# Performance work log

Hardware: AMD Instinct MI355X
Metric: run time of the kernel (lower is better)

## Reference

```python
import jax, jax.numpy as jnp
import numpy as np

NUM_NODES = 1024
K = 16384
G = 128

def setup_inputs() -> dict:
    key = jax.random.key(0)
    k1, k2, k3 = jax.random.split(key, 3)
    x = jax.random.normal(k1, (G, NUM_NODES, 64), dtype=jnp.float32)
    # original draws fresh xavier-uniform embeddings inside forward; we
    # materialize equivalent random embeddings here (only ordering matters).
    emb_s = jax.random.normal(k2, (G, NUM_NODES, 1), dtype=jnp.float32)
    emb_t = jax.random.normal(k3, (G, 1, NUM_NODES), dtype=jnp.float32)
    return {"x": x, "emb_s": emb_s, "emb_t": emb_t}

def reference(x, emb_s, emb_t):
    num_graphs = x.shape[0]
    n = NUM_NODES
    # rank-1 outer product adjacency: [G, N, N]
    adj = emb_s * emb_t  # broadcast (G,N,1)*(G,1,N)
    # mask diagonal with -inf
    diag = jnp.eye(n, dtype=bool)
    adj = jnp.where(diag[None, :, :], -jnp.inf, adj)
    # global top-k over flattened N*N per graph
    adj_flat = adj.reshape(num_graphs, n * n)
    _, indices = jax.lax.top_k(adj_flat, K)  # [G, K]
    # scatter ones at selected positions
    out_flat = jnp.zeros((num_graphs, n * n), dtype=adj.dtype)
    rows = jnp.arange(num_graphs)[:, None]
    out_flat = out_flat.at[rows, indices].set(1.0)
    return out_flat.reshape(num_graphs, n, n)
```

## Files before the change

### kernel.cpp

```cpp
#include <hip/hip_runtime.h>
#include <stdint.h>

#define NNODES 1024
#define NGRAPH 128
#define TOPK   16384
#define EQCAP  4096

typedef float vfloat4 __attribute__((ext_vector_type(4)));

__device__ __forceinline__ uint32_t fkey(float x) {
    uint32_t u = __float_as_uint(x);
    return (u & 0x80000000u) ? ~u : (u | 0x80000000u);
}
__device__ __forceinline__ float inv_fkey(uint32_t k) {
    uint32_t u = (k & 0x80000000u) ? (k & 0x7FFFFFFFu) : ~k;
    return __uint_as_float(u);
}

__global__ __launch_bounds__(NNODES)
void select_kernel(const float* __restrict__ s, const float* __restrict__ t,
                   uint32_t* __restrict__ Tout, uint32_t* __restrict__ Rout,
                   uint32_t* __restrict__ eqCntG, uint32_t* __restrict__ eqIdxG) {
    const int g = blockIdx.x, i = threadIdx.x;
    __shared__ uint64_t spk[NNODES];
    __shared__ float    tvs[NNODES];
    __shared__ uint32_t wsum[16];
    __shared__ uint32_t sLo, sHi, sDir, sEqCnt;
    __shared__ uint32_t sEqList[EQCAP];

    const float tv_i = t[g * NNODES + i];
    spk[i] = ((uint64_t)fkey(tv_i) << 16) | (uint32_t)i;
    if (i == 0) { sLo = 0u; sHi = 0xFFFFFFFFu; sEqCnt = 0u; }

    for (int k = 2; k <= NNODES; k <<= 1) {
        for (int j = k >> 1; j > 0; j >>= 1) {
            __syncthreads();
            int partner = i ^ j;
            if (partner > i) {
                bool asc = ((i & k) == 0);
                uint64_t a = spk[i], b = spk[partner];
                if ((a > b) == asc) { spk[i] = b; spk[partner] = a; }
            }
        }
    }
    __syncthreads();
    tvs[i] = inv_fkey((uint32_t)(spk[i] >> 16));

    const float sv = s[g * NNODES + i];
    const bool sneg = (__float_as_uint(sv) >> 31) != 0;
    const uint32_t kdiag = fkey(sv * tv_i);
    __syncthreads();

    auto srchRange = [&](uint32_t cand, int lo_, int hi_) -> int {
        while (lo_ < hi_) {
            int mid = (lo_ + hi_) >> 1;
            bool pred = fkey(sv * tvs[mid]) > cand;
            bool goLeft = sneg ? !pred : pred;
            if (goLeft) hi_ = mid; else lo_ = mid + 1;
        }
        return lo_;
    };

    int rlo = 0, rhi = NNODES;
    uint32_t cntHi = 0u;

    for (int it = 0; it < 33; ++it) {
        const uint32_t lo = sLo, hi = sHi;
        const uint32_t mid = lo + ((hi - lo) >> 1);
        const int b = srchRange(mid, rlo, rhi);
        uint32_t c = sneg ? (uint32_t)b : (uint32_t)(NNODES - b);
        if (kdiag > mid) c--;
        uint32_t r = c;
        for (int off = 32; off; off >>= 1) r += __shfl_down(r, off);
        if ((i & 63) == 0) wsum[i >> 6] = r;
        __syncthreads();
        if (i == 0 && lo < hi) {
            uint32_t tot = 0;
            for (int w = 0; w < 16; ++w) tot += wsum[w];
            if (tot < TOPK) { sHi = mid; sDir = 0u; cntHi = tot; }
            else            { sLo = mid + 1; sDir = 1u; }
        }
        __syncthreads();
        if (lo < hi) {
            if (sDir == 0u) { if (!sneg) rhi = b; else rlo = b; }
            else            { if (!sneg) rlo = b; else rhi = b; }
        }
    }
    const uint32_t T = sLo;
    if (i == 0) { Tout[g] = T; Rout[g] = TOPK - cntHi; }

    auto bound = [&](bool ge) -> int {
        int lo_ = 0, hi_ = NNODES;
        while (lo_ < hi_) {
            int mid = (lo_ + hi_) >> 1;
            uint32_t k = fkey(sv * tvs[mid]);
            bool pred = ge ? (k >= T) : (k > T);
            bool goLeft = sneg ? !pred : pred;
            if (goLeft) hi_ = mid; else lo_ = mid + 1;
        }
        return lo_;
    };
    int e0, e1;
    if (!sneg) { e0 = bound(true);  e1 = bound(false); }
    else       { e0 = bound(false); e1 = bound(true);  }
    for (int p = e0; p < e1; ++p) {
        uint32_t j = (uint32_t)(spk[p] & 0xFFFFu);
        if ((int)j == i) continue;
        uint32_t slot = atomicAdd(&sEqCnt, 1u);
        if (slot < EQCAP) sEqList[slot] = (uint32_t)(i * NNODES) + j;
    }
    __syncthreads();
    uint32_t E = sEqCnt; if (E > EQCAP) E = EQCAP;
    if (i == 0) eqCntG[g] = E;
    for (uint32_t p = i; p < E; p += NNODES) eqIdxG[g * EQCAP + p] = sEqList[p];
}

__global__ __launch_bounds__(256)
void write_kernel(const float* __restrict__ s, const float* __restrict__ t,
                  const uint32_t* __restrict__ Tin, const uint32_t* __restrict__ Rin,
                  const uint32_t* __restrict__ eqCntG, const uint32_t* __restrict__ eqIdxG,
                  float* __restrict__ out) {
    const int b = blockIdx.x;
    const int g = b >> 10, i = b & 1023;
    const uint32_t T = Tin[g];
    const float sv = s[(size_t)g * NNODES + i];
    const vfloat4 tv = ((const vfloat4*)(t + (size_t)g * NNODES))[threadIdx.x];
    const int j0 = threadIdx.x * 4;
    const uint32_t k0 = fkey(sv * tv.x), k1 = fkey(sv * tv.y);
    const uint32_t k2 = fkey(sv * tv.z), k3 = fkey(sv * tv.w);
    vfloat4 o;
    o.x = (k0 > T && (j0 + 0) != i) ? 1.0f : 0.0f;
    o.y = (k1 > T && (j0 + 1) != i) ? 1.0f : 0.0f;
    o.z = (k2 > T && (j0 + 2) != i) ? 1.0f : 0.0f;
    o.w = (k3 > T && (j0 + 3) != i) ? 1.0f : 0.0f;
    if (k0 == T || k1 == T || k2 == T || k3 == T) {
        uint32_t E = eqCntG[g]; if (E > EQCAP) E = EQCAP;
        const uint32_t R = Rin[g];
        const uint32_t* eq = eqIdxG + (size_t)g * EQCAP;
        const uint32_t kk[4] = {k0, k1, k2, k3};
        #pragma unroll
        for (int q = 0; q < 4; ++q) {
            const uint32_t j = j0 + q;
            if (kk[q] == T && (int)j != i) {
                const uint32_t f = (uint32_t)i * NNODES + j;
                uint32_t rank = 0;
                for (uint32_t e2 = 0; e2 < E; ++e2) rank += (eq[e2] < f) ? 1u : 0u;
                if (rank < R) ((float*)&o)[q] = 1.0f;
            }
        }
    }
    ((vfloat4*)(out + (size_t)g * NNODES * NNODES + (size_t)i * NNODES))[threadIdx.x] = o;
}

extern "C" void kernel_launch(void* const* d_in, const int* in_sizes, int n_in,
                              void* d_out, int out_size, void* d_ws, size_t ws_size,
                              hipStream_t stream) {
    const float* s = (const float*)d_in[1];
    const float* t = (const float*)d_in[2];
    float* out = (float*)d_out;

    char* ws = (char*)d_ws;
    uint32_t* Tbuf  = (uint32_t*)ws; ws += (size_t)NGRAPH * 4;
    uint32_t* Rbuf  = (uint32_t*)ws; ws += (size_t)NGRAPH * 4;
    uint32_t* eqCnt = (uint32_t*)ws; ws += (size_t)NGRAPH * 4;
    uint32_t* eqIdx = (uint32_t*)ws; ws += (size_t)NGRAPH * EQCAP * 4;

    select_kernel<<<NGRAPH, NNODES, 0, stream>>>(s, t, Tbuf, Rbuf, eqCnt, eqIdx);
    write_kernel<<<NGRAPH * NNODES, 256, 0, stream>>>(s, t, Tbuf, Rbuf, eqCnt, eqIdx, out);
}
```

Baseline: 137.2 us.

## Use wave barriers for intra-wave sort stages and narrow threshold search bounds

In the bitonic sort, block-wide __syncthreads is replaced by a wavefront barrier when the compare stride stays within one 64-lane wave. This cuts the number of block-level barriers. The threshold bisection now starts from a tighter range: the lower bound is the minimum over rows of each row's 17th-largest product, and the upper bound is the maximum product. The loop also exits early once the range collapses, so fewer iterations, each with two block barriers, are needed. Both changes rely on the wave64 execution model and on the bound argument that every row has at least 16 off-diagonal entries at or above its 17th-largest value.

Result: no change. 136.5 us (-0.6%).

```diff
diff --git a/kernel.cpp b/kernel.cpp
--- a/kernel.cpp
+++ b/kernel.cpp
@@ -16,6 +16,10 @@
     uint32_t u = (k & 0x80000000u) ? (k & 0x7FFFFFFFu) : ~k;
     return __uint_as_float(u);
 }
+__device__ __forceinline__ void wavefence() {
+    __builtin_amdgcn_wave_barrier();
+    asm volatile("" ::: "memory");
+}
 
 __global__ __launch_bounds__(NNODES)
 void select_kernel(const float* __restrict__ s, const float* __restrict__ t,
@@ -24,17 +28,18 @@
     const int g = blockIdx.x, i = threadIdx.x;
     __shared__ uint64_t spk[NNODES];
     __shared__ float    tvs[NNODES];
-    __shared__ uint32_t wsum[16];
+    __shared__ uint32_t wsum[16], wsum2[16];
     __shared__ uint32_t sLo, sHi, sDir, sEqCnt;
     __shared__ uint32_t sEqList[EQCAP];
 
     const float tv_i = t[g * NNODES + i];
     spk[i] = ((uint64_t)fkey(tv_i) << 16) | (uint32_t)i;
-    if (i == 0) { sLo = 0u; sHi = 0xFFFFFFFFu; sEqCnt = 0u; }
+    if (i == 0) sEqCnt = 0u;
 
     for (int k = 2; k <= NNODES; k <<= 1) {
         for (int j = k >> 1; j > 0; j >>= 1) {
-            __syncthreads();
+            if ((j >= 64) || (j == 32 && k > 64)) __syncthreads();
+            else                                  wavefence();
             int partner = i ^ j;
             if (partner > i) {
                 bool asc = ((i & k) == 0);
@@ -51,6 +56,26 @@
     const uint32_t kdiag = fkey(sv * tv_i);
     __syncthreads();
 
+    {
+        uint32_t m = fkey(sv * tvs[sneg ? 0 : (NNODES - 1)]);
+        uint32_t n = fkey(sv * tvs[sneg ? 16 : (NNODES - 17)]);
+        for (int off = 32; off; off >>= 1) {
+            uint32_t mm = __shfl_down(m, off); if (mm > m) m = mm;
+            uint32_t nn = __shfl_down(n, off); if (nn < n) n = nn;
+        }
+        if ((i & 63) == 0) { wsum[i >> 6] = m; wsum2[i >> 6] = n; }
+        __syncthreads();
+        if (i == 0) {
+            uint32_t ub = 0u, lb = 0xFFFFFFFFu;
+            for (int w = 0; w < 16; ++w) {
+                if (wsum[w]  > ub) ub = wsum[w];
+                if (wsum2[w] < lb) lb = wsum2[w];
+            }
+            sLo = lb; sHi = ub;
+        }
+        __syncthreads();
+    }
+
     auto srchRange = [&](uint32_t cand, int lo_, int hi_) -> int {
         while (lo_ < hi_) {
             int mid = (lo_ + hi_) >> 1;
@@ -66,6 +91,7 @@
 
     for (int it = 0; it < 33; ++it) {
         const uint32_t lo = sLo, hi = sHi;
+        if (lo >= hi) break;
         const uint32_t mid = lo + ((hi - lo) >> 1);
         const int b = srchRange(mid, rlo, rhi);
         uint32_t c = sneg ? (uint32_t)b : (uint32_t)(NNODES - b);
@@ -74,17 +100,15 @@
         for (int off = 32; off; off >>= 1) r += __shfl_down(r, off);
         if ((i & 63) == 0) wsum[i >> 6] = r;
         __syncthreads();
-        if (i == 0 && lo < hi) {
+        if (i == 0) {
             uint32_t tot = 0;
             for (int w = 0; w < 16; ++w) tot += wsum[w];
             if (tot < TOPK) { sHi = mid; sDir = 0u; cntHi = tot; }
             else            { sLo = mid + 1; sDir = 1u; }
         }
         __syncthreads();
-        if (lo < hi) {
-            if (sDir == 0u) { if (!sneg) rhi = b; else rlo = b; }
-            else            { if (!sneg) rlo = b; else rhi = b; }
-        }
+        if (sDir == 0u) { if (!sneg) rhi = b; else rlo = b; }
+        else            { if (!sneg) rlo = b; else rhi = b; }
     }
     const uint32_t T = sLo;
     if (i == 0) { Tout[g] = T; Rout[g] = TOPK - cntHi; }
```
